# Performance work log

Hardware: AMD Instinct MI355X
Metric: run time of the kernel (lower is better)

## Reference

```python
import jax, jax.numpy as jnp
import numpy as np

TS = 16      # tile size
ST = 4       # stride
IN = 224     # image size
G = (IN - TS) // ST + 1   # 53 tiles per side
L = G * G                 # 2809 tiles
CH = [3 * L, 3 * L // 4, 3 * L // 16, 3 * L // 4, 3 * L]  # [8427,2106,526,2106,8427]

# torch_dct-style unnormalized DCT-II matrix and its exact inverse (DCT-III based)
_n = np.arange(TS)
_k = np.arange(TS)[:, None]
_C = np.cos(np.pi * (2 * _n[None, :] + 1) * _k / (2 * TS))  # [k, n]
D_DCT = jnp.asarray(2.0 * _C, jnp.float32)                   # dct: y = D @ x
_w = np.ones(TS); _w[0] = 0.5
D_IDCT = jnp.asarray((_C.T * _w[None, :]) / TS, jnp.float32) # idct: x = Dinv @ y

# gather/scatter indices for unfold/fold (constants)
IH = (np.arange(G) * ST)[:, None] + np.arange(TS)[None, :]   # [G, TS]
IW = IH


def setup_inputs() -> dict:
    key = jax.random.key(0)
    ks = jax.random.split(key, 9)
    x = jax.random.normal(ks[0], (8, 3, IN, IN), jnp.float32)
    def lin(k, o, c):
        return jax.random.normal(k, (o, c), jnp.float32) * 0.02
    return {
        'x': x,
        'w1': lin(ks[1], CH[1], CH[0]), 'b1': jnp.zeros((CH[1],), jnp.float32),
        'w2': lin(ks[2], CH[2], CH[1]), 'b2': jnp.zeros((CH[2],), jnp.float32),
        'w3': lin(ks[3], CH[3], CH[2]), 'b3': jnp.zeros((CH[3],), jnp.float32),
        'w4': lin(ks[4], CH[4], CH[3]), 'b4': jnp.zeros((CH[4],), jnp.float32),
    }


def _forward(x, w1, b1, w2, b2, w3, b3, w4, b4):
    b = x.shape[0]
    # unfold: gather overlapping 16x16 patches -> [b, 3, G, G, TS, TS]
    p = x[:, :, IH[:, None, :, None], IW[None, :, None, :]]
    # torch ordering after permute+reshape: channel index = l*3 + c
    tiles = p.transpose(0, 2, 3, 1, 4, 5).reshape(b, 3 * L, TS, TS)
    # 2D DCT (unnormalized DCT-II along last two dims)
    dct_tiles = jnp.einsum('km,ln,bcmn->bckl', D_DCT, D_DCT, tiles)
    # mask net: stack of 1x1 convs over the tile-channel dim
    h = dct_tiles / (TS * TS)
    h = jax.nn.relu(jnp.einsum('oc,bchw->bohw', w1, h) + b1[:, None, None])
    h = jax.nn.relu(jnp.einsum('oc,bchw->bohw', w2, h) + b2[:, None, None])
    h = jax.nn.relu(jnp.einsum('oc,bchw->bohw', w3, h) + b3[:, None, None])
    masks = jax.nn.sigmoid(jnp.einsum('oc,bchw->bohw', w4, h) + b4[:, None, None])
    clean_dct = masks * dct_tiles
    # 2D inverse DCT
    clean_tiles = jnp.einsum('mk,nl,bckl->bcmn', D_IDCT, D_IDCT, clean_dct)
    # fold: scatter-add patches back with overlap
    ct = clean_tiles.reshape(b, G, G, 3, TS, TS).transpose(0, 3, 1, 2, 4, 5)
    out = jnp.zeros((b, 3, IN, IN), x.dtype)
    out = out.at[:, :, IH[:, None, :, None], IW[None, :, None, :]].add(ct)
    # scale = fold(unfold(ones)): per-pixel overlap counts (recomputed per call, as in source)
    scale = jnp.zeros((IN, IN), x.dtype)
    scale = scale.at[IH[:, None, :, None], IW[None, :, None, :]].add(
        jnp.ones((G, G, TS, TS), x.dtype))
    return out / scale


def reference(x, w1, b1, w2, b2, w3, b3, w4, b4):
    return _forward(x, w1, b1, w2, b2, w3, b3, w4, b4)
```

## Files before the change

### kernel.cpp

```cpp
#include <hip/hip_runtime.h>
#include <stdint.h>

constexpr int INSZ = 224;
constexpr int GD   = 53;
constexpr int C0R = 8427, C1R = 2106, C2R = 526;
constexpr int C0P = 8448, C1P = 2304, C2P = 640;
constexpr int NTOK = 2048;
constexpr int CROW = GD * 16;

typedef __attribute__((ext_vector_type(4))) float f32x4;
typedef __attribute__((ext_vector_type(8))) short bf16x8;

constexpr float CT[64] = {
  1.00000000f,  0.99518473f,  0.98078528f,  0.95694034f,
  0.92387953f,  0.88192126f,  0.83146961f,  0.77301045f,
  0.70710678f,  0.63439328f,  0.55557023f,  0.47139674f,
  0.38268343f,  0.29028468f,  0.19509032f,  0.09801714f,
  0.00000000f, -0.09801714f, -0.19509032f, -0.29028468f,
 -0.38268343f, -0.47139674f, -0.55557023f, -0.63439328f,
 -0.70710678f, -0.77301045f, -0.83146961f, -0.88192126f,
 -0.92387953f, -0.95694034f, -0.98078528f, -0.99518473f,
 -1.00000000f, -0.99518473f, -0.98078528f, -0.95694034f,
 -0.92387953f, -0.88192126f, -0.83146961f, -0.77301045f,
 -0.70710678f, -0.63439328f, -0.55557023f, -0.47139674f,
 -0.38268343f, -0.29028468f, -0.19509032f, -0.09801714f,
 -0.00000000f,  0.09801714f,  0.19509032f,  0.29028468f,
  0.38268343f,  0.47139674f,  0.55557023f,  0.63439328f,
  0.70710678f,  0.77301045f,  0.83146961f,  0.88192126f,
  0.92387953f,  0.95694034f,  0.98078528f,  0.99518473f
};
constexpr float Dfwd(int k, int n) { return 2.0f * CT[((2 * n + 1) * k) & 63]; }
constexpr float Dinv(int n, int k) { return CT[((2 * n + 1) * k) & 63] * (k == 0 ? 0.03125f : 0.0625f); }

constexpr int TRS_R = 20, TRS_T = 336;
constexpr int TRS_SZ = 15 * TRS_T + 15 * TRS_R + 16;

__device__ __forceinline__ unsigned short f2bf(float f) {
  union { float f; unsigned u; } v; v.f = f;
  return (unsigned short)((v.u + 0x7FFFu + ((v.u >> 16) & 1u)) >> 16);
}
__device__ __forceinline__ float bf2f(unsigned short b) {
  union { unsigned u; float f; } v; v.u = ((unsigned)b) << 16;
  return v.f;
}

__device__ __forceinline__ void gload_lds16(const void* g, void* l) {
  __builtin_amdgcn_global_load_lds(
      (__attribute__((address_space(1))) unsigned int*)(uintptr_t)g,
      (__attribute__((address_space(3))) unsigned int*)(unsigned int)(uintptr_t)l,
      16, 0, 0);
}

__device__ __forceinline__ void xcd_tile(int& bx, int& by) {
  const int gx = gridDim.x, gy = gridDim.y;
  const int nwg = gx * gy;
  const int bid = blockIdx.y * gx + blockIdx.x;
  const int cpx = nwg >> 3;
  const int l = (bid & 7) * cpx + (bid >> 3);
  const int stripe = gy << 2;
  const int bxg = l / stripe;
  const int r = l - bxg * stripe;
  const int rem = gx - (bxg << 2);
  const int w = rem < 4 ? rem : 4;
  by = r / w;
  bx = (bxg << 2) + (r - by * w);
}

constexpr int CV1_GPR = C0P / 8;
constexpr int CV1_TOT = C1P * CV1_GPR;
__global__ __launch_bounds__(256)
void cvt_pad8_w1(const float* __restrict__ src, unsigned short* __restrict__ dst) {
  const int i = blockIdx.x * 256 + threadIdx.x;
  if (i >= CV1_TOT) return;
  const int m = i / CV1_GPR;
  const int k0 = (i - m * CV1_GPR) * 8;
  const float* sr = src + (size_t)m * C0R + k0;
  const bool mok = (m < C1R);
  unsigned short h[8];
#pragma unroll
  for (int e = 0; e < 8; ++e)
    h[e] = f2bf((mok && k0 + e < C0R) ? sr[e] : 0.f);
  uint4 pk;
  pk.x = (unsigned)h[0] | ((unsigned)h[1] << 16);
  pk.y = (unsigned)h[2] | ((unsigned)h[3] << 16);
  pk.z = (unsigned)h[4] | ((unsigned)h[5] << 16);
  pk.w = (unsigned)h[6] | ((unsigned)h[7] << 16);
  *(uint4*)&dst[(size_t)m * C0P + k0] = pk;
}

constexpr int CV8_1 = C2P * C1P / 8;
constexpr int CV8_2 = CV8_1 + C1P * C2P / 8;
constexpr int CV8_T = CV8_2 + C0P * C1P / 8;
__global__ __launch_bounds__(256)
void cvt_pad8_all(const float* __restrict__ w2, const float* __restrict__ w3,
                  const float* __restrict__ w4, unsigned short* __restrict__ d2,
                  unsigned short* __restrict__ d3, unsigned short* __restrict__ d4) {
  const int i = blockIdx.x * 256 + threadIdx.x;
  const float* src; unsigned short* dst;
  int m, k0, Kreal, Mreal, Kp;
  if (i < CV8_1) {
    const int gpr = C1P / 8;
    m = i / gpr; k0 = (i - m * gpr) * 8;
    src = w2; dst = d2; Mreal = C2R; Kreal = C1R; Kp = C1P;
  } else if (i < CV8_2) {
    const int j = i - CV8_1;
    const int gpr = C2P / 8;
    m = j / gpr; k0 = (j - m * gpr) * 8;
    src = w3; dst = d3; Mreal = C1R; Kreal = C2R; Kp = C2P;
  } else {
    const int j = i - CV8_2;
    const int gpr = C1P / 8;
    m = j / gpr; k0 = (j - m * gpr) * 8;
    src = w4; dst = d4; Mreal = C0R; Kreal = C1R; Kp = C1P;
  }
  const float* sr = src + (size_t)m * Kreal + k0;
  const bool mok = (m < Mreal);
  unsigned short h[8];
#pragma unroll
  for (int e = 0; e < 8; ++e)
    h[e] = f2bf((mok && k0 + e < Kreal) ? sr[e] : 0.f);
  uint4 pk;
  pk.x = (unsigned)h[0] | ((unsigned)h[1] << 16);
  pk.y = (unsigned)h[2] | ((unsigned)h[3] << 16);
  pk.z = (unsigned)h[4] | ((unsigned)h[5] << 16);
  pk.w = (unsigned)h[6] | ((unsigned)h[7] << 16);
  *(uint4*)&dst[(size_t)m * Kp + k0] = pk;
}

__global__ __launch_bounds__(256)
void dct_h0(const float* __restrict__ x, unsigned short* __restrict__ H0) {
  __shared__ float trp[TRS_SZ];
  __shared__ unsigned short hst[256 * 64];
  const int tid = threadIdx.x;
  const int b   = blockIdx.y;
  const int c0  = blockIdx.x * 64;
  const int t = tid >> 4, q = tid & 15;

  for (int g = 0; g < 4; ++g) {
    const int c = c0 + g * 16 + t;
    float p[16];
    {
      float4 v0{}, v1{}, v2{}, v3{};
      if (c < C0R) {
        const int ch = c % 3, gw = (c / 3) % GD, gh = c / (3 * GD);
        const float* xr = x + ((size_t)(b * 3 + ch) * INSZ + (gh * 4 + q)) * INSZ + gw * 4;
        v0 = *(const float4*)(xr);      v1 = *(const float4*)(xr + 4);
        v2 = *(const float4*)(xr + 8);  v3 = *(const float4*)(xr + 12);
      }
      p[0]=v0.x; p[1]=v0.y; p[2]=v0.z; p[3]=v0.w;
      p[4]=v1.x; p[5]=v1.y; p[6]=v1.z; p[7]=v1.w;
      p[8]=v2.x; p[9]=v2.y; p[10]=v2.z; p[11]=v2.w;
      p[12]=v3.x; p[13]=v3.y; p[14]=v3.z; p[15]=v3.w;
    }
    float r[16];
#pragma unroll
    for (int k = 0; k < 16; ++k) {
      float s = 0.f;
#pragma unroll
      for (int n = 0; n < 16; ++n) s += p[n] * Dfwd(k, n);
      r[k] = s;
    }
    float* wr = &trp[t * TRS_T + q * TRS_R];
#pragma unroll
    for (int k = 0; k < 16; k += 4)
      *(float4*)(wr + k) = make_float4(r[k], r[k+1], r[k+2], r[k+3]);
    __syncthreads();
    const int j = q;
    float rr[16];
#pragma unroll
    for (int i = 0; i < 16; ++i) rr[i] = trp[t * TRS_T + i * TRS_R + j];
#pragma unroll
    for (int k = 0; k < 16; ++k) {
      float s = 0.f;
#pragma unroll
      for (int i = 0; i < 16; ++i) s += rr[i] * Dfwd(k, i);
      hst[(k * 16 + j) * 64 + g * 16 + t] = f2bf(s * (1.f / 256.f));
    }
    __syncthreads();
  }
  const size_t base = ((size_t)b * 256) * C0P + c0;
#pragma unroll
  for (int i = 0; i < 8; ++i) {
    const int s = i * 256 + tid;
    const int kl = s >> 3, c16 = s & 7;
    *(uint4*)&H0[base + (size_t)kl * C0P + c16 * 8] = *(const uint4*)&hst[kl * 64 + c16 * 8];
  }
}

template<int ACT, int OUT_NM, int SPLITK>
__global__ __launch_bounds__(512, 2)
void gemm256(const unsigned short* __restrict__ W, const unsigned short* __restrict__ Ht,
             const float* __restrict__ bias, void* __restrict__ outp,
             int ldo, int Kp, int chunkK) {
  __shared__ unsigned short As[4][8192];
  __shared__ unsigned short Bs[4][8192];
  int bx, by; xcd_tile(bx, by);
  const int m0 = bx * 256, n0 = by * 256;
  const int tid = threadIdx.x;
  const int w = tid >> 6, lane = tid & 63;
  const int wr = w >> 2, wc = w & 3;
  const int lhi = lane >> 4, llo = lane & 15;
  const int kbase = SPLITK ? blockIdx.z * chunkK : 0;
  const int nkt = chunkK >> 5;

  const int srow = tid >> 2;
  const int slgc = ((tid & 3) ^ ((srow >> 1) & 3)) * 8;

  f32x4 acc[8][4];
#pragma unroll
  for (int i = 0; i < 8; ++i)
#pragma unroll
    for (int j = 0; j < 4; ++j) acc[i][j] = f32x4{0.f, 0.f, 0.f, 0.f};

  auto STAGE_A = [&](int kt, int buf) {
    const int kb = kbase + kt * 32 + slgc;
    gload_lds16(W + (size_t)(m0 + srow) * Kp + kb,       &As[buf][w * 512]);
    gload_lds16(W + (size_t)(m0 + 128 + srow) * Kp + kb, &As[buf][4096 + w * 512]);
  };
  auto STAGE_B = [&](int kt, int buf) {
    const int kb = kbase + kt * 32 + slgc;
    gload_lds16(Ht + (size_t)(n0 + srow) * Kp + kb,       &Bs[buf][w * 512]);
    gload_lds16(Ht + (size_t)(n0 + 128 + srow) * Kp + kb, &Bs[buf][4096 + w * 512]);
  };

  STAGE_A(0, 0); STAGE_B(0, 0);
  if (nkt > 1) { STAGE_A(1, 1); STAGE_B(1, 1); }
  if (nkt > 2) { STAGE_A(2, 2); STAGE_B(2, 2); }

  for (int kt = 0; kt < nkt; ++kt) {
    const int buf  = kt & 3;
    const int sbuf = (kt + 3) & 3;
    if (kt + 3 <= nkt)      asm volatile("s_waitcnt vmcnt(8)" ::: "memory");
    else if (kt + 2 == nkt) asm volatile("s_waitcnt vmcnt(4)" ::: "memory");
    else                    asm volatile("s_waitcnt vmcnt(0)" ::: "memory");
    __builtin_amdgcn_s_barrier();
    __builtin_amdgcn_sched_barrier(0);

    bf16x8 af[4], bfr[4];
#pragma unroll
    for (int mi = 0; mi < 4; ++mi) {
      const int row = wr * 128 + mi * 16 + llo;
      af[mi] = *(const bf16x8*)(&As[buf][row * 32 + ((lhi ^ ((row >> 1) & 3)) << 3)]);
    }
#pragma unroll
    for (int ni = 0; ni < 4; ++ni) {
      const int row = wc * 64 + ni * 16 + llo;
      bfr[ni] = *(const bf16x8*)(&Bs[buf][row * 32 + ((lhi ^ ((row >> 1) & 3)) << 3)]);
    }
    if (kt + 3 < nkt) STAGE_A(kt + 3, sbuf);
    __builtin_amdgcn_s_setprio(1);
#pragma unroll
    for (int mi = 0; mi < 4; ++mi)
#pragma unroll
      for (int ni = 0; ni < 4; ++ni)
        acc[mi][ni] = OUT_NM
          ? __builtin_amdgcn_mfma_f32_16x16x32_bf16(bfr[ni], af[mi], acc[mi][ni], 0, 0, 0)
          : __builtin_amdgcn_mfma_f32_16x16x32_bf16(af[mi], bfr[ni], acc[mi][ni], 0, 0, 0);
    __builtin_amdgcn_s_setprio(0);
#pragma unroll
    for (int mi = 0; mi < 4; ++mi) {
      const int row = wr * 128 + 64 + mi * 16 + llo;
      af[mi] = *(const bf16x8*)(&As[buf][row * 32 + ((lhi ^ ((row >> 1) & 3)) << 3)]);
    }
    if (kt + 3 < nkt) STAGE_B(kt + 3, sbuf);
    __builtin_amdgcn_s_setprio(1);
#pragma unroll
    for (int mi = 0; mi < 4; ++mi)
#pragma unroll
      for (int ni = 0; ni < 4; ++ni)
        acc[4 + mi][ni] = OUT_NM
          ? __builtin_amdgcn_mfma_f32_16x16x32_bf16(bfr[ni], af[mi], acc[4 + mi][ni], 0, 0, 0)
          : __builtin_amdgcn_mfma_f32_16x16x32_bf16(af[mi], bfr[ni], acc[4 + mi][ni], 0, 0, 0);
    __builtin_amdgcn_s_setprio(0);
  }

  if (SPLITK) {
    float* pz = (float*)outp + (size_t)blockIdx.z * ((size_t)NTOK * ldo);
#pragma unroll
    for (int mh = 0; mh < 2; ++mh)
#pragma unroll
      for (int mi = 0; mi < 4; ++mi) {
        const int mg = m0 + wr * 128 + mh * 64 + mi * 16 + llo;
#pragma unroll
        for (int ni = 0; ni < 4; ++ni) {
          const int ng = n0 + wc * 64 + ni * 16 + lhi * 4;
#pragma unroll
          for (int r = 0; r < 4; ++r)
            pz[(size_t)(ng + r) * ldo + mg] = acc[mh * 4 + mi][ni][r];
        }
      }
  } else {
    unsigned short* out = (unsigned short*)outp;
#pragma unroll
    for (int mh = 0; mh < 2; ++mh)
#pragma unroll
      for (int mi = 0; mi < 4; ++mi) {
        const int mgb = m0 + wr * 128 + mh * 64 + mi * 16 + lhi * 4;
#pragma unroll
        for (int ni = 0; ni < 4; ++ni) {
          const int ng = n0 + wc * 64 + ni * 16 + llo;
#pragma unroll
          for (int r = 0; r < 4; ++r) {
            const int mg = mgb + r;
            float v = acc[mh * 4 + mi][ni][r] + bias[mg];
            if (ACT == 1) v = fmaxf(v, 0.f);
            else if (ACT == 2) v = 1.f / (1.f + expf(-v));
            out[(size_t)mg * ldo + ng] = f2bf(v);
          }
        }
      }
  }
}

template<int OUT_NM>
__device__ __forceinline__ void gemm_core(
    const unsigned short* __restrict__ W, const unsigned short* __restrict__ Ht,
    unsigned short (*As)[128 * 32], unsigned short (*Bs)[128 * 32],
    int m0, int n0, int Kp, int kbase, int nkt, int w, int lane, f32x4 acc[4][4]) {
  const int wr = w >> 1, wc = w & 1;
  const int lhi = lane >> 4, llo = lane & 15;

  const int chunk0 = w * 64 + lane;
  const int row0 = chunk0 >> 2, kc0 = chunk0 & 3;
  const int kcg0 = kc0 ^ ((row0 >> 1) & 3);
  const int chunk1 = 256 + w * 64 + lane;
  const int row1 = chunk1 >> 2, kc1 = chunk1 & 3;
  const int kcg1 = kc1 ^ ((row1 >> 1) & 3);

  auto STAGE = [&](int kt, int sel) {
    const int kb = kbase + kt * 32;
    gload_lds16(W  + (size_t)(m0 + row0) * Kp + kb + kcg0 * 8, &As[sel][(w * 64) * 8]);
    gload_lds16(Ht + (size_t)(n0 + row0) * Kp + kb + kcg0 * 8, &Bs[sel][(w * 64) * 8]);
    gload_lds16(W  + (size_t)(m0 + row1) * Kp + kb + kcg1 * 8, &As[sel][(256 + w * 64) * 8]);
    gload_lds16(Ht + (size_t)(n0 + row1) * Kp + kb + kcg1 * 8, &Bs[sel][(256 + w * 64) * 8]);
  };

  STAGE(0, 0);
  if (nkt > 1) STAGE(1, 1);

  int cur = 0, nxt = 1, nx2 = 2;
  for (int kt = 0; kt < nkt; ++kt) {
    if (kt + 1 < nkt) {
      asm volatile("s_waitcnt vmcnt(4)" ::: "memory");
      __builtin_amdgcn_s_barrier();
      __builtin_amdgcn_sched_barrier(0);
      if (kt + 2 < nkt) STAGE(kt + 2, nx2);
    } else {
      asm volatile("s_waitcnt vmcnt(0)" ::: "memory");
      __builtin_amdgcn_s_barrier();
      __builtin_amdgcn_sched_barrier(0);
    }
    bf16x8 af[4], bfr[4];
#pragma unroll
    for (int mi = 0; mi < 4; ++mi) {
      const int row = wr * 64 + mi * 16 + llo;
      af[mi] = *(const bf16x8*)(&As[cur][row * 32 + (lhi ^ ((row >> 1) & 3)) * 8]);
    }
#pragma unroll
    for (int ni = 0; ni < 4; ++ni) {
      const int row = wc * 64 + ni * 16 + llo;
      bfr[ni] = *(const bf16x8*)(&Bs[cur][row * 32 + (lhi ^ ((row >> 1) & 3)) * 8]);
    }
#pragma unroll
    for (int mi = 0; mi < 4; ++mi)
#pragma unroll
      for (int ni = 0; ni < 4; ++ni) {
        if (OUT_NM)
          acc[mi][ni] = __builtin_amdgcn_mfma_f32_16x16x32_bf16(bfr[ni], af[mi], acc[mi][ni], 0, 0, 0);
        else
          acc[mi][ni] = __builtin_amdgcn_mfma_f32_16x16x32_bf16(af[mi], bfr[ni], acc[mi][ni], 0, 0, 0);
      }
    const int tmp = cur; cur = nxt; nxt = nx2; nx2 = tmp;
  }
}

__global__ __launch_bounds__(256)
void gemm_splitk(const unsigned short* __restrict__ W, const unsigned short* __restrict__ Ht,
                 float* __restrict__ part, int ldo , int Kp, int chunkK) {
  __shared__ unsigned short As[3][128 * 32];
  __shared__ unsigned short Bs[3][128 * 32];
  int bx, by; xcd_tile(bx, by);
  const int z = blockIdx.z;
  const int tid = threadIdx.x;
  const int w = tid >> 6, lane = tid & 63;
  const int m0 = bx * 128, n0 = by * 128;
  const int wr = w >> 1, wc = w & 1;
  const int lhi = lane >> 4, llo = lane & 15;

  f32x4 acc[4][4];
#pragma unroll
  for (int i = 0; i < 4; ++i)
#pragma unroll
    for (int j = 0; j < 4; ++j) acc[i][j] = f32x4{0.f, 0.f, 0.f, 0.f};

  gemm_core<1>(W, Ht, As, Bs, m0, n0, Kp, z * chunkK, chunkK >> 5, w, lane, acc);

  float* pz = part + (size_t)z * NTOK * ldo;
#pragma unroll
  for (int mi = 0; mi < 4; ++mi) {
    const int mg = m0 + wr * 64 + mi * 16 + llo;
#pragma unroll
    for (int ni = 0; ni < 4; ++ni) {
      const int ng = n0 + wc * 64 + ni * 16 + lhi * 4;
#pragma unroll
      for (int r = 0; r < 4; ++r)
        pz[(size_t)(ng + r) * ldo + mg] = acc[mi][ni][r];
    }
  }
}

__global__ __launch_bounds__(256)
void gemm_splitk_mn(const unsigned short* __restrict__ W, const unsigned short* __restrict__ Ht,
                    float* __restrict__ part, int Kp, int chunkK) {
  __shared__ unsigned short As[3][128 * 32];
  __shared__ unsigned short Bs[3][128 * 32];
  int bx, by; xcd_tile(bx, by);
  const int z = blockIdx.z;
  const int tid = threadIdx.x;
  const int w = tid >> 6, lane = tid & 63;
  const int m0 = bx * 128, n0 = by * 128;
  const int wr = w >> 1, wc = w & 1;
  const int lhi = lane >> 4, llo = lane & 15;
  const int Mloc = gridDim.x * 128;

  f32x4 acc[4][4];
#pragma unroll
  for (int i = 0; i < 4; ++i)
#pragma unroll
    for (int j = 0; j < 4; ++j) acc[i][j] = f32x4{0.f, 0.f, 0.f, 0.f};

  gemm_core<0>(W, Ht, As, Bs, m0, n0, Kp, z * chunkK, chunkK >> 5, w, lane, acc);

  float* pz = part + (size_t)z * Mloc * NTOK;
#pragma unroll
  for (int mi = 0; mi < 4; ++mi) {
    const int mlb = m0 + wr * 64 + mi * 16 + lhi * 4;
#pragma unroll
    for (int ni = 0; ni < 4; ++ni) {
      const int ng = n0 + wc * 64 + ni * 16 + llo;
#pragma unroll
      for (int r = 0; r < 4; ++r)
        pz[(size_t)(mlb + r) * NTOK + ng] = acc[mi][ni][r];
    }
  }
}

__global__ __launch_bounds__(256)
void reduce_sig(const float* __restrict__ part, const float* __restrict__ bias,
                unsigned short* __restrict__ msk, int mbase, int Mloc, int nch) {
  const int i8 = blockIdx.x * 256 + threadIdx.x;
  const int total = Mloc * NTOK / 8;
  if (i8 >= total) return;
  const size_t off = (size_t)i8 * 8;
  const int ml = (int)(off >> 11);
  float s[8] = {0.f, 0.f, 0.f, 0.f, 0.f, 0.f, 0.f, 0.f};
  for (int z = 0; z < nch; ++z) {
    const float4 v0 = *(const float4*)(part + (size_t)z * Mloc * NTOK + off);
    const float4 v1 = *(const float4*)(part + (size_t)z * Mloc * NTOK + off + 4);
    s[0] += v0.x; s[1] += v0.y; s[2] += v0.z; s[3] += v0.w;
    s[4] += v1.x; s[5] += v1.y; s[6] += v1.z; s[7] += v1.w;
  }
  const int mg = mbase + ml;
  const float b = (mg < C0R) ? bias[mg] : 0.f;
  unsigned short h[8];
#pragma unroll
  for (int e = 0; e < 8; ++e)
    h[e] = f2bf(1.f / (1.f + expf(-(s[e] + b))));
  uint4 pk;
  pk.x = (unsigned)h[0] | ((unsigned)h[1] << 16);
  pk.y = (unsigned)h[2] | ((unsigned)h[3] << 16);
  pk.z = (unsigned)h[4] | ((unsigned)h[5] << 16);
  pk.w = (unsigned)h[6] | ((unsigned)h[7] << 16);
  *(uint4*)&msk[(size_t)mg * NTOK + (off & 2047)] = pk;
}

__global__ __launch_bounds__(256)
void reduce_act(const float* __restrict__ part, const float* __restrict__ bias,
                unsigned short* __restrict__ out, int Mp, int Mreal, int nch) {
  const int i8 = blockIdx.x * 256 + threadIdx.x;
  const int total = NTOK * Mp / 8;
  if (i8 >= total) return;
  const size_t off = (size_t)i8 * 8;
  const int m0 = (int)(off % Mp);
  float s[8] = {0.f, 0.f, 0.f, 0.f, 0.f, 0.f, 0.f, 0.f};
  for (int z = 0; z < nch; ++z) {
    const float4 v0 = *(const float4*)(part + (size_t)z * NTOK * Mp + off);
    const float4 v1 = *(const float4*)(part + (size_t)z * NTOK * Mp + off + 4);
    s[0] += v0.x; s[1] += v0.y; s[2] += v0.z; s[3] += v0.w;
    s[4] += v1.x; s[5] += v1.y; s[6] += v1.z; s[7] += v1.w;
  }
  unsigned short h[8];
#pragma unroll
  for (int e = 0; e < 8; ++e) {
    const float b = (m0 + e < Mreal) ? bias[m0 + e] : 0.f;
    h[e] = f2bf(fmaxf(s[e] + b, 0.f));
  }
  uint4 pk;
  pk.x = (unsigned)h[0] | ((unsigned)h[1] << 16);
  pk.y = (unsigned)h[2] | ((unsigned)h[3] << 16);
  pk.z = (unsigned)h[4] | ((unsigned)h[5] << 16);
  pk.w = (unsigned)h[6] | ((unsigned)h[7] << 16);
  *(uint4*)&out[off] = pk;
}

__global__ __launch_bounds__(256)
void mask_idct(const float* __restrict__ x, const unsigned short* __restrict__ masks,
               unsigned short* __restrict__ clean) {
  __shared__ float trp[TRS_SZ];
  const int tid = threadIdx.x;
  const int b   = blockIdx.y;
  const int c0  = blockIdx.x * 16;
  const int t = tid >> 4, q = tid & 15;
  const int c = c0 + t;
  const bool valid = (c < C0R);
  const int ch = c % 3, gw = (c / 3) % GD, gh = c / (3 * GD);

  float p[16];
  {
    float4 v0{}, v1{}, v2{}, v3{};
    if (valid) {
      const float* xr = x + ((size_t)(b * 3 + ch) * INSZ + (gh * 4 + q)) * INSZ + gw * 4;
      v0 = *(const float4*)(xr);      v1 = *(const float4*)(xr + 4);
      v2 = *(const float4*)(xr + 8);  v3 = *(const float4*)(xr + 12);
    }
    p[0]=v0.x; p[1]=v0.y; p[2]=v0.z; p[3]=v0.w;
    p[4]=v1.x; p[5]=v1.y; p[6]=v1.z; p[7]=v1.w;
    p[8]=v2.x; p[9]=v2.y; p[10]=v2.z; p[11]=v2.w;
    p[12]=v3.x; p[13]=v3.y; p[14]=v3.z; p[15]=v3.w;
  }
  float r[16];
#pragma unroll
  for (int k = 0; k < 16; ++k) {
    float s = 0.f;
#pragma unroll
    for (int n = 0; n < 16; ++n) s += p[n] * Dfwd(k, n);
    r[k] = s;
  }
  {
    float* wr = &trp[t * TRS_T + q * TRS_R];
#pragma unroll
    for (int k = 0; k < 16; k += 4)
      *(float4*)(wr + k) = make_float4(r[k], r[k+1], r[k+2], r[k+3]);
  }
  __syncthreads();
  const int j = q;
  float rr[16];
#pragma unroll
  for (int i = 0; i < 16; ++i) rr[i] = trp[t * TRS_T + i * TRS_R + j];
  float cd[16];
  const unsigned short* mrow = masks + (size_t)c * NTOK + (size_t)b * 256 + j;
#pragma unroll
  for (int k = 0; k < 16; ++k) {
    float s = 0.f;
#pragma unroll
    for (int i = 0; i < 16; ++i) s += rr[i] * Dfwd(k, i);
    const float mv = valid ? bf2f(mrow[k * 16]) : 0.f;
    cd[k] = s * mv;
  }
  float t3[16];
#pragma unroll
  for (int m = 0; m < 16; ++m) {
    float s = 0.f;
#pragma unroll
    for (int k = 0; k < 16; ++k) s += cd[k] * Dinv(m, k);
    t3[m] = s;
  }
  __syncthreads();
  {
    float* wr = &trp[t * TRS_T + j * TRS_R];
#pragma unroll
    for (int m = 0; m < 16; m += 4)
      *(float4*)(wr + m) = make_float4(t3[m], t3[m+1], t3[m+2], t3[m+3]);
  }
  __syncthreads();
  float tr[16];
#pragma unroll
  for (int l = 0; l < 16; ++l) tr[l] = trp[t * TRS_T + l * TRS_R + q];
  if (valid) {
    unsigned pk[8];
#pragma unroll
    for (int n2 = 0; n2 < 8; ++n2) {
      float s0 = 0.f, s1 = 0.f;
#pragma unroll
      for (int l = 0; l < 16; ++l) {
        s0 += tr[l] * Dinv(2 * n2, l);
        s1 += tr[l] * Dinv(2 * n2 + 1, l);
      }
      pk[n2] = (unsigned)f2bf(s0) | ((unsigned)f2bf(s1) << 16);
    }
    unsigned short* dst = clean +
        ((((size_t)(b * 3 + ch) * GD + gh) * 16 + q) * CROW) + gw * 16;
    uint4* d4 = (uint4*)dst;
    d4[0] = make_uint4(pk[0], pk[1], pk[2], pk[3]);
    d4[1] = make_uint4(pk[4], pk[5], pk[6], pk[7]);
  }
}

__global__ void overlap_add(const unsigned short* __restrict__ clean, float* __restrict__ out) {
  const int px = blockIdx.x * 256 + threadIdx.x;
  if (px >= 8 * 3 * 224 * 224) return;
  const int j = px % 224;
  const int i = (px / 224) % 224;
  const int bc = px / (224 * 224);
  const int ilo = i - 15;
  const int ghlo = ilo > 0 ? (ilo + 3) >> 2 : 0;
  const int ghhi = (i >> 2) < 52 ? (i >> 2) : 52;
  const int jlo = j - 15;
  const int gwlo = jlo > 0 ? (jlo + 3) >> 2 : 0;
  const int gwhi = (j >> 2) < 52 ? (j >> 2) : 52;
  float sum = 0.f;
  for (int gh = ghlo; gh <= ghhi; ++gh) {
    const int r = i - gh * 4;
    const unsigned short* row = clean + (((size_t)bc * GD + gh) * 16 + r) * CROW;
    for (int gw = gwlo; gw <= gwhi; ++gw)
      sum += bf2f(row[j + 12 * gw]);
  }
  const int cnt = (ghhi - ghlo + 1) * (gwhi - gwlo + 1);
  out[px] = sum / (float)cnt;
}

extern "C" void kernel_launch(void* const* d_in, const int* in_sizes, int n_in,
                              void* d_out, int out_size, void* d_ws, size_t ws_size,
                              hipStream_t stream) {
  const float* x  = (const float*)d_in[0];
  const float* w1 = (const float*)d_in[1];
  const float* b1 = (const float*)d_in[2];
  const float* w2 = (const float*)d_in[3];
  const float* b2 = (const float*)d_in[4];
  const float* w3 = (const float*)d_in[5];
  const float* b3 = (const float*)d_in[6];
  const float* w4 = (const float*)d_in[7];
  const float* b4 = (const float*)d_in[8];
  float* out = (float*)d_out;
  char* ws = (char*)d_ws;

  const size_t OFF_A = 0;
  const size_t OFF_B = 38928384;
  const size_t OFF_C = 73531392;

  unsigned short* wb1   = (unsigned short*)(ws + OFF_A);
  unsigned short* wb4   = (unsigned short*)(ws + OFF_A);
  unsigned short* clean = (unsigned short*)(ws + OFF_A);

  unsigned short* H0v = (unsigned short*)(ws + OFF_B);
  unsigned short* Y1  = (unsigned short*)(ws + OFF_B);
  unsigned short* wb2 = (unsigned short*)(ws + OFF_B + 9437184);
  unsigned short* wb3 = (unsigned short*)(ws + OFF_B + 12386304);
  unsigned short* Y2  = (unsigned short*)(ws + OFF_B + 15335424);
  unsigned short* msk = (unsigned short*)(ws + OFF_B);

  float* pt1 = (float*)(ws + OFF_C);
  float* pt2 = (float*)(ws + OFF_C);
  float* pt3 = (float*)(ws + OFF_C);
  float* pt4 = (float*)(ws + OFF_C);
  unsigned short* Y3 = (unsigned short*)(ws + OFF_C + 37748736);

  cvt_pad8_w1<<<dim3(CV1_TOT / 256), 256, 0, stream>>>(w1, wb1);
  dct_h0<<<dim3(C0P / 64, 8), 256, 0, stream>>>(x, H0v);

  gemm256<0, 1, 1><<<dim3(C1P / 256, NTOK / 256, 3), 512, 0, stream>>>(
      wb1, H0v, nullptr, pt1, C1P, C0P, 2816);
  reduce_act<<<dim3(NTOK * C1P / 8 / 256), 256, 0, stream>>>(pt1, b1, Y1, C1P, C1R, 3);

  cvt_pad8_all<<<dim3(CV8_T / 256), 256, 0, stream>>>(w2, w3, w4, wb2, wb3, wb4);

  gemm_splitk<<<dim3(C2P / 128, NTOK / 128, 4), 256, 0, stream>>>(wb2, Y1, pt2, C2P, C1P, 576);
  reduce_act<<<dim3(NTOK * C2P / 8 / 256), 256, 0, stream>>>(pt2, b2, Y2, C2P, C2R, 4);

  gemm_splitk<<<dim3(C1P / 128, NTOK / 128, 2), 256, 0, stream>>>(wb3, Y2, pt3, C1P, C2P, 320);
  reduce_act<<<dim3(NTOK * C1P / 8 / 256), 256, 0, stream>>>(pt3, b3, Y3, C1P, C1R, 2);

  gemm256<2, 0, 0><<<dim3(32, NTOK / 256), 512, 0, stream>>>(
      wb4, Y3, b4, msk, NTOK, C1P, C1P);
  gemm_splitk_mn<<<dim3(2, NTOK / 128, 4), 256, 0, stream>>>(
      wb4 + (size_t)8192 * C1P, Y3, pt4, C1P, 576);
  reduce_sig<<<dim3(256 * NTOK / 8 / 256), 256, 0, stream>>>(pt4, b4, msk, 8192, 256, 4);

  mask_idct<<<dim3((C0R + 15) / 16, 8), 256, 0, stream>>>(x, msk, clean);

  overlap_add<<<dim3((8 * 3 * 224 * 224 + 255) / 256), 256, 0, stream>>>(clean, out);
}
```

Baseline: 395.1 us.

## Merge prep kernels, fuse reduce with weight conversion, trim padded K ranges

The w1 bf16 conversion and the DCT kernel are merged into one launch, selected by block index. The first split-K reduction plus ReLU is merged with the w2/w3/w4 conversion kernel. The GEMM K-chunk sizes are cut to skip zero-padded K regions (2112 instead of 2304 for layer 4, 544x4 and 288x2 for layers 2 and 3), and the layer-4 tail split-K goes from 4 splits to 3. This removes launch overhead and wasted MACs on padding, but it relies on the padding being exactly zero and on the chunk sizes covering every real K.

After: 390.5 us. No clear change (-1.2%).

```diff
diff --git a/kernel.cpp b/kernel.cpp
--- a/kernel.cpp
+++ b/kernel.cpp
@@ -7,6 +7,10 @@
 constexpr int C0P = 8448, C1P = 2304, C2P = 640;
 constexpr int NTOK = 2048;
 constexpr int CROW = GD * 16;
+constexpr int K1EFF = 2112;
+constexpr int K2EFF = 2176;
+constexpr int K3EFF = 576;
+constexpr int K4TEF = 2112;
 
 typedef __attribute__((ext_vector_type(4))) float f32x4;
 typedef __attribute__((ext_vector_type(8))) short bf16x8;
@@ -67,35 +71,127 @@
 }
 
 constexpr int CV1_GPR = C0P / 8;
-constexpr int CV1_TOT = C1P * CV1_GPR;
+constexpr int P1_CVB  = C1P * CV1_GPR / 256;
+constexpr int P1_DCTX = C0P / 64;
 __global__ __launch_bounds__(256)
-void cvt_pad8_w1(const float* __restrict__ src, unsigned short* __restrict__ dst) {
-  const int i = blockIdx.x * 256 + threadIdx.x;
-  if (i >= CV1_TOT) return;
-  const int m = i / CV1_GPR;
-  const int k0 = (i - m * CV1_GPR) * 8;
-  const float* sr = src + (size_t)m * C0R + k0;
-  const bool mok = (m < C1R);
-  unsigned short h[8];
-#pragma unroll
-  for (int e = 0; e < 8; ++e)
-    h[e] = f2bf((mok && k0 + e < C0R) ? sr[e] : 0.f);
-  uint4 pk;
-  pk.x = (unsigned)h[0] | ((unsigned)h[1] << 16);
-  pk.y = (unsigned)h[2] | ((unsigned)h[3] << 16);
-  pk.z = (unsigned)h[4] | ((unsigned)h[5] << 16);
-  pk.w = (unsigned)h[6] | ((unsigned)h[7] << 16);
-  *(uint4*)&dst[(size_t)m * C0P + k0] = pk;
-}
-
+void prep1(const float* __restrict__ w1, unsigned short* __restrict__ wb1,
+           const float* __restrict__ x, unsigned short* __restrict__ H0) {
+  __shared__ float trp[TRS_SZ];
+  __shared__ unsigned short hst[256 * 64];
+  const int tid = threadIdx.x;
+
+  if ((int)blockIdx.x < P1_CVB) {
+    const int i = blockIdx.x * 256 + tid;
+    const int m = i / CV1_GPR;
+    const int k0 = (i - m * CV1_GPR) * 8;
+    const float* sr = w1 + (size_t)m * C0R + k0;
+    const bool mok = (m < C1R);
+    unsigned short h[8];
+#pragma unroll
+    for (int e = 0; e < 8; ++e)
+      h[e] = f2bf((mok && k0 + e < C0R) ? sr[e] : 0.f);
+    uint4 pk;
+    pk.x = (unsigned)h[0] | ((unsigned)h[1] << 16);
+    pk.y = (unsigned)h[2] | ((unsigned)h[3] << 16);
+    pk.z = (unsigned)h[4] | ((unsigned)h[5] << 16);
+    pk.w = (unsigned)h[6] | ((unsigned)h[7] << 16);
+    *(uint4*)&wb1[(size_t)m * C0P + k0] = pk;
+    return;
+  }
+  const int flat = blockIdx.x - P1_CVB;
+  const int bxx = flat % P1_DCTX;
+  const int b   = flat / P1_DCTX;
+  const int c0  = bxx * 64;
+  const int t = tid >> 4, q = tid & 15;
+
+  for (int g = 0; g < 4; ++g) {
+    const int c = c0 + g * 16 + t;
+    float p[16];
+    {
+      float4 v0{}, v1{}, v2{}, v3{};
+      if (c < C0R) {
+        const int ch = c % 3, gw = (c / 3) % GD, gh = c / (3 * GD);
+        const float* xr = x + ((size_t)(b * 3 + ch) * INSZ + (gh * 4 + q)) * INSZ + gw * 4;
+        v0 = *(const float4*)(xr);      v1 = *(const float4*)(xr + 4);
+        v2 = *(const float4*)(xr + 8);  v3 = *(const float4*)(xr + 12);
+      }
+      p[0]=v0.x; p[1]=v0.y; p[2]=v0.z; p[3]=v0.w;
+      p[4]=v1.x; p[5]=v1.y; p[6]=v1.z; p[7]=v1.w;
+      p[8]=v2.x; p[9]=v2.y; p[10]=v2.z; p[11]=v2.w;
+      p[12]=v3.x; p[13]=v3.y; p[14]=v3.z; p[15]=v3.w;
+    }
+    float r[16];
+#pragma unroll
+    for (int k = 0; k < 16; ++k) {
+      float s = 0.f;
+#pragma unroll
+      for (int n = 0; n < 16; ++n) s += p[n] * Dfwd(k, n);
+      r[k] = s;
+    }
+    float* wr = &trp[t * TRS_T + q * TRS_R];
+#pragma unroll
+    for (int k = 0; k < 16; k += 4)
+      *(float4*)(wr + k) = make_float4(r[k], r[k+1], r[k+2], r[k+3]);
+    __syncthreads();
+    const int j = q;
+    float rr[16];
+#pragma unroll
+    for (int i = 0; i < 16; ++i) rr[i] = trp[t * TRS_T + i * TRS_R + j];
+#pragma unroll
+    for (int k = 0; k < 16; ++k) {
+      float s = 0.f;
+#pragma unroll
+      for (int i = 0; i < 16; ++i) s += rr[i] * Dfwd(k, i);
+      hst[(k * 16 + j) * 64 + g * 16 + t] = f2bf(s * (1.f / 256.f));
+    }
+    __syncthreads();
+  }
+  const size_t base = ((size_t)b * 256) * C0P + c0;
+#pragma unroll
+  for (int i = 0; i < 8; ++i) {
+    const int s = i * 256 + tid;
+    const int kl = s >> 3, c16 = s & 7;
+    *(uint4*)&H0[base + (size_t)kl * C0P + c16 * 8] = *(const uint4*)&hst[kl * 64 + c16 * 8];
+  }
+}
+
+constexpr int M1_RB = NTOK * C1P / 8 / 256;
 constexpr int CV8_1 = C2P * C1P / 8;
 constexpr int CV8_2 = CV8_1 + C1P * C2P / 8;
 constexpr int CV8_T = CV8_2 + C0P * C1P / 8;
 __global__ __launch_bounds__(256)
-void cvt_pad8_all(const float* __restrict__ w2, const float* __restrict__ w3,
-                  const float* __restrict__ w4, unsigned short* __restrict__ d2,
-                  unsigned short* __restrict__ d3, unsigned short* __restrict__ d4) {
-  const int i = blockIdx.x * 256 + threadIdx.x;
+void mid1(const float* __restrict__ part, const float* __restrict__ b1,
+          unsigned short* __restrict__ Y1,
+          const float* __restrict__ w2, const float* __restrict__ w3,
+          const float* __restrict__ w4, unsigned short* __restrict__ d2,
+          unsigned short* __restrict__ d3, unsigned short* __restrict__ d4) {
+  const int tid = threadIdx.x;
+  if ((int)blockIdx.x < M1_RB) {
+    const int i8 = blockIdx.x * 256 + tid;
+    const size_t off = (size_t)i8 * 8;
+    const int m0 = (int)(off % C1P);
+    float s[8] = {0.f, 0.f, 0.f, 0.f, 0.f, 0.f, 0.f, 0.f};
+    for (int z = 0; z < 3; ++z) {
+      const float4 v0 = *(const float4*)(part + (size_t)z * NTOK * C1P + off);
+      const float4 v1 = *(const float4*)(part + (size_t)z * NTOK * C1P + off + 4);
+      s[0] += v0.x; s[1] += v0.y; s[2] += v0.z; s[3] += v0.w;
+      s[4] += v1.x; s[5] += v1.y; s[6] += v1.z; s[7] += v1.w;
+    }
+    unsigned short h[8];
+#pragma unroll
+    for (int e = 0; e < 8; ++e) {
+      const float b = (m0 + e < C1R) ? b1[m0 + e] : 0.f;
+      h[e] = f2bf(fmaxf(s[e] + b, 0.f));
+    }
+    uint4 pk;
+    pk.x = (unsigned)h[0] | ((unsigned)h[1] << 16);
+    pk.y = (unsigned)h[2] | ((unsigned)h[3] << 16);
+    pk.z = (unsigned)h[4] | ((unsigned)h[5] << 16);
+    pk.w = (unsigned)h[6] | ((unsigned)h[7] << 16);
+    *(uint4*)&Y1[off] = pk;
+    return;
+  }
+  const int i = (blockIdx.x - M1_RB) * 256 + tid;
   const float* src; unsigned short* dst;
   int m, k0, Kreal, Mreal, Kp;
   if (i < CV8_1) {
@@ -125,66 +221,6 @@
   pk.z = (unsigned)h[4] | ((unsigned)h[5] << 16);
   pk.w = (unsigned)h[6] | ((unsigned)h[7] << 16);
   *(uint4*)&dst[(size_t)m * Kp + k0] = pk;
-}
-
-__global__ __launch_bounds__(256)
-void dct_h0(const float* __restrict__ x, unsigned short* __restrict__ H0) {
-  __shared__ float trp[TRS_SZ];
-  __shared__ unsigned short hst[256 * 64];
-  const int tid = threadIdx.x;
-  const int b   = blockIdx.y;
-  const int c0  = blockIdx.x * 64;
-  const int t = tid >> 4, q = tid & 15;
-
-  for (int g = 0; g < 4; ++g) {
-    const int c = c0 + g * 16 + t;
-    float p[16];
-    {
-      float4 v0{}, v1{}, v2{}, v3{};
-      if (c < C0R) {
-        const int ch = c % 3, gw = (c / 3) % GD, gh = c / (3 * GD);
-        const float* xr = x + ((size_t)(b * 3 + ch) * INSZ + (gh * 4 + q)) * INSZ + gw * 4;
-        v0 = *(const float4*)(xr);      v1 = *(const float4*)(xr + 4);
-        v2 = *(const float4*)(xr + 8);  v3 = *(const float4*)(xr + 12);
-      }
-      p[0]=v0.x; p[1]=v0.y; p[2]=v0.z; p[3]=v0.w;
-      p[4]=v1.x; p[5]=v1.y; p[6]=v1.z; p[7]=v1.w;
-      p[8]=v2.x; p[9]=v2.y; p[10]=v2.z; p[11]=v2.w;
-      p[12]=v3.x; p[13]=v3.y; p[14]=v3.z; p[15]=v3.w;
-    }
-    float r[16];
-#pragma unroll
-    for (int k = 0; k < 16; ++k) {
-      float s = 0.f;
-#pragma unroll
-      for (int n = 0; n < 16; ++n) s += p[n] * Dfwd(k, n);
-      r[k] = s;
-    }
-    float* wr = &trp[t * TRS_T + q * TRS_R];
-#pragma unroll
-    for (int k = 0; k < 16; k += 4)
-      *(float4*)(wr + k) = make_float4(r[k], r[k+1], r[k+2], r[k+3]);
-    __syncthreads();
-    const int j = q;
-    float rr[16];
-#pragma unroll
-    for (int i = 0; i < 16; ++i) rr[i] = trp[t * TRS_T + i * TRS_R + j];
-#pragma unroll
-    for (int k = 0; k < 16; ++k) {
-      float s = 0.f;
-#pragma unroll
-      for (int i = 0; i < 16; ++i) s += rr[i] * Dfwd(k, i);
-      hst[(k * 16 + j) * 64 + g * 16 + t] = f2bf(s * (1.f / 256.f));
-    }
-    __syncthreads();
-  }
-  const size_t base = ((size_t)b * 256) * C0P + c0;
-#pragma unroll
-  for (int i = 0; i < 8; ++i) {
-    const int s = i * 256 + tid;
-    const int kl = s >> 3, c16 = s & 7;
-    *(uint4*)&H0[base + (size_t)kl * C0P + c16 * 8] = *(const uint4*)&hst[kl * 64 + c16 * 8];
-  }
 }
 
 template<int ACT, int OUT_NM, int SPLITK>
@@ -655,26 +691,25 @@
   float* pt4 = (float*)(ws + OFF_C);
   unsigned short* Y3 = (unsigned short*)(ws + OFF_C + 37748736);
 
-  cvt_pad8_w1<<<dim3(CV1_TOT / 256), 256, 0, stream>>>(w1, wb1);
-  dct_h0<<<dim3(C0P / 64, 8), 256, 0, stream>>>(x, H0v);
+  prep1<<<dim3(P1_CVB + P1_DCTX * 8), 256, 0, stream>>>(w1, wb1, x, H0v);
 
   gemm256<0, 1, 1><<<dim3(C1P / 256, NTOK / 256, 3), 512, 0, stream>>>(
       wb1, H0v, nullptr, pt1, C1P, C0P, 2816);
-  reduce_act<<<dim3(NTOK * C1P / 8 / 256), 256, 0, stream>>>(pt1, b1, Y1, C1P, C1R, 3);
-
-  cvt_pad8_all<<<dim3(CV8_T / 256), 256, 0, stream>>>(w2, w3, w4, wb2, wb3, wb4);
-
-  gemm_splitk<<<dim3(C2P / 128, NTOK / 128, 4), 256, 0, stream>>>(wb2, Y1, pt2, C2P, C1P, 576);
+
+  mid1<<<dim3(M1_RB + CV8_T / 256), 256, 0, stream>>>(
+      pt1, b1, Y1, w2, w3, w4, wb2, wb3, wb4);
+
+  gemm_splitk<<<dim3(C2P / 128, NTOK / 128, 4), 256, 0, stream>>>(wb2, Y1, pt2, C2P, C1P, 544);
   reduce_act<<<dim3(NTOK * C2P / 8 / 256), 256, 0, stream>>>(pt2, b2, Y2, C2P, C2R, 4);
 
-  gemm_splitk<<<dim3(C1P / 128, NTOK / 128, 2), 256, 0, stream>>>(wb3, Y2, pt3, C1P, C2P, 320);
+  gemm_splitk<<<dim3(C1P / 128, NTOK / 128, 2), 256, 0, stream>>>(wb3, Y2, pt3, C1P, C2P, 288);
   reduce_act<<<dim3(NTOK * C1P / 8 / 256), 256, 0, stream>>>(pt3, b3, Y3, C1P, C1R, 2);
 
   gemm256<2, 0, 0><<<dim3(32, NTOK / 256), 512, 0, stream>>>(
-      wb4, Y3, b4, msk, NTOK, C1P, C1P);
-  gemm_splitk_mn<<<dim3(2, NTOK / 128, 4), 256, 0, stream>>>(
-      wb4 + (size_t)8192 * C1P, Y3, pt4, C1P, 576);
-  reduce_sig<<<dim3(256 * NTOK / 8 / 256), 256, 0, stream>>>(pt4, b4, msk, 8192, 256, 4);
+      wb4, Y3, b4, msk, NTOK, C1P, K1EFF);
+  gemm_splitk_mn<<<dim3(2, NTOK / 128, 3), 256, 0, stream>>>(
+      wb4 + (size_t)8192 * C1P, Y3, pt4, C1P, 704);
+  reduce_sig<<<dim3(256 * NTOK / 8 / 256), 256, 0, stream>>>(pt4, b4, msk, 8192, 256, 3);
 
   mask_idct<<<dim3((C0R + 15) / 16, 8), 256, 0, stream>>>(x, msk, clean);
 
```
